# Kernel optimization log

Measured on AMD Instinct MI355X. Metric: run time of the kernel, lower is better.

## Reference

```python
import jax, jax.numpy as jnp
import numpy as np

NUM_CLASSES = 80
TOP_K = 200
CONF_T = 0.05
NMS_T = 0.5
CROP = 300.0
A = 49104
B = 8
NEG = -1.0  # dead-score sentinel; real scores are sigmoid outputs in (0,1)


def setup_inputs() -> dict:
    key = jax.random.key(0)
    k1, k2, k3, k4, k5, k6 = jax.random.split(key, 6)
    # structured, plausible anchors in (ymin, xmin, ymax, xmax), pixel coords
    yc = jax.random.uniform(k1, (A,)) * CROP
    xc = jax.random.uniform(k2, (A,)) * CROP
    h = 10.0 + jax.random.uniform(k5, (A,)) * 90.0
    w = 10.0 + jax.random.uniform(k6, (A,)) * 90.0
    anchors = jnp.stack([yc - h / 2, xc - w / 2, yc + h / 2, xc + w / 2], axis=-1)
    confidences = jax.random.normal(k3, (B, A, NUM_CLASSES + 1), dtype=jnp.float32)
    regressions = jax.random.normal(k4, (B, A, 4), dtype=jnp.float32) * 0.1
    return {"confidences": confidences, "regressions": regressions, "anchors": anchors}


def _decode(regressions, anchors):
    yca = (anchors[:, 0] + anchors[:, 2]) / 2
    xca = (anchors[:, 1] + anchors[:, 3]) / 2
    ha = anchors[:, 2] - anchors[:, 0]
    wa = anchors[:, 3] - anchors[:, 1]
    w = jnp.exp(regressions[..., 3]) * wa
    h = jnp.exp(regressions[..., 2]) * ha
    yc = regressions[..., 0] * ha + yca
    xc = regressions[..., 1] * wa + xca
    # clamp exactly as the original: min-clamp on xmin/ymin, max-clamp on xmax/ymax
    xmin = jnp.maximum(xc - w / 2, 0.0) / CROP
    ymin = jnp.maximum(yc - h / 2, 0.0) / CROP
    xmax = jnp.minimum(xc + w / 2, CROP - 1.0) / CROP
    ymax = jnp.minimum(yc + h / 2, CROP - 1.0) / CROP
    return jnp.stack([xmin, ymin, xmax, ymax], axis=-1)  # [B,A,4] (x1,y1,x2,y2)


def _iou_one_to_many(box, boxes):
    x1 = jnp.maximum(box[0], boxes[:, 0])
    y1 = jnp.maximum(box[1], boxes[:, 1])
    x2 = jnp.minimum(box[2], boxes[:, 2])
    y2 = jnp.minimum(box[3], boxes[:, 3])
    inter = jnp.maximum(x2 - x1, 0.0) * jnp.maximum(y2 - y1, 0.0)
    area_b = (box[2] - box[0]) * (box[3] - box[1])
    areas = (boxes[:, 2] - boxes[:, 0]) * (boxes[:, 3] - boxes[:, 1])
    union = area_b + areas - inter
    return jnp.where(union > 0, inter / union, 0.0)


def _nms_image(boxes, probs):
    # boxes: [A,4], probs: [A,C] (sigmoid, background stripped)
    scores = jnp.max(probs, axis=1)
    classes = jnp.argmax(probs, axis=1)
    valid = scores > CONF_T
    # batched_nms trick: offset boxes per class so cross-class IoU is 0
    offset = classes.astype(boxes.dtype) * (jnp.max(boxes) + 1.0)
    boxes_o = boxes + offset[:, None]
    live = jnp.where(valid, scores, NEG)

    def body(live, _):
        idx = jnp.argmax(live)
        keep = live[idx] > 0.0
        iou = _iou_one_to_many(boxes_o[idx], boxes_o)
        live = jnp.where(keep & (iou > NMS_T), NEG, live)
        live = live.at[idx].set(NEG)
        return live, (idx, keep)

    _, (idxs, keeps) = jax.lax.scan(body, live, None, length=TOP_K)
    cls_k = classes[idxs]          # [TOP_K]
    sc_k = scores[idxs]            # [TOP_K]
    bx_k = boxes[idxs]             # [TOP_K,4]
    # per-class slot = rank among kept detections of the same class (keep order is score-descending)
    onehot = (cls_k[:, None] == jnp.arange(NUM_CLASSES)[None, :]) & keeps[:, None]
    slot = jnp.cumsum(onehot, axis=0)[jnp.arange(TOP_K), cls_k] - 1
    rows = jnp.where(keeps, cls_k + 1, NUM_CLASSES + 1)  # OOB row when dropped
    slot = jnp.where(keeps, slot, TOP_K)                 # OOB col when dropped
    vals = jnp.concatenate([sc_k[:, None], bx_k], axis=1)  # [TOP_K,5]
    out = jnp.zeros((NUM_CLASSES + 1, TOP_K, 5), boxes.dtype)
    return out.at[rows, slot].set(vals, mode="drop")


def reference(confidences, regressions, anchors):
    probs = jax.nn.sigmoid(confidences[:, :, 1:])
    boxes = _decode(regressions, anchors)
    return jax.vmap(_nms_image)(boxes, probs)  # [B, C+1, TOP_K, 5]
```

## Files before the change

kernel.cpp:

```cpp
#include <hip/hip_runtime.h>
#include <stdint.h>

#define NCLS 80
#define TOPK 200
#define CONF_T 0.05f
#define CONF_BITS 0x3D4CCCCDu
#define CROPF 300.0f
#define NA 49104
#define NB 8
#define NSEL 256
#define MKEYS 4096
#define APB 64
#define T1 256
#define CHUNK (APB * 81)
#define NGRP (NA / 16)
#define MROW 5
#define OUTFLO ((NCLS + 1) * TOPK * 5)
#define NBLK1 ((NB * NA) / APB)
#define BASE13 125542u
#define NBINS 4512

__device__ __forceinline__ void decode_box(const float4 rg, const float4 an,
                                           float& x1, float& y1, float& x2, float& y2) {
    float yca = (an.x + an.z) * 0.5f;
    float xca = (an.y + an.w) * 0.5f;
    float ha = an.z - an.x;
    float wa = an.w - an.y;
    float w = expf(rg.w) * wa;
    float h = expf(rg.z) * ha;
    float yc = rg.x * ha + yca;
    float xc = rg.y * wa + xca;
    x1 = fmaxf(xc - w * 0.5f, 0.0f) / CROPF;
    y1 = fmaxf(yc - h * 0.5f, 0.0f) / CROPF;
    x2 = fminf(xc + w * 0.5f, CROPF - 1.0f) / CROPF;
    y2 = fminf(yc + h * 0.5f, CROPF - 1.0f) / CROPF;
}

__device__ __forceinline__ float rlf(float v, int l) {
    return __int_as_float(__builtin_amdgcn_readlane(__float_as_int(v), l));
}

__global__ __launch_bounds__(T1) void phase1_kernel(
    const float* __restrict__ conf, const float* __restrict__ reg,
    const float* __restrict__ anch, unsigned long long* __restrict__ key64,
    float4* __restrict__ boxes, float2* __restrict__ gm2,
    float* __restrict__ outz)
{
    __shared__ float lds[CHUNK];
    const int blk = blockIdx.x, t = threadIdx.x;

    {
        const int gid = blk * T1 + t;
        constexpr int TOT4 = NB * OUTFLO / 4;
        if (gid < TOT4)
            reinterpret_cast<float4*>(outz)[gid] = make_float4(0.f, 0.f, 0.f, 0.f);
    }

    const float4* src = reinterpret_cast<const float4*>(conf + (size_t)blk * CHUNK);
    float4* dst = reinterpret_cast<float4*>(lds);
    for (int i = t; i < CHUNK / 4; i += T1) dst[i] = src[i];
    __syncthreads();

    const int la = t >> 2, sub = t & 3;
    const int quad = blk * APB + la;
    const float* crow = lds + la * 81;
    float best = -3.0e38f; int bc = 255;
    #pragma unroll
    for (int k = 0; k < 20; ++k) {
        int c = 1 + sub + 4 * k;
        float v = crow[c];
        if (v > best) { best = v; bc = c; }
    }
    for (int m = 1; m <= 2; m <<= 1) {
        float ov = __shfl_xor(best, m);
        int oc = __shfl_xor(bc, m);
        if (ov > best || (ov == best && oc < bc)) { best = ov; bc = oc; }
    }
    unsigned long long key = 0ull;
    float bmaxl = 0.0f;
    if (sub == 0) {
        int a = quad % NA;
        float s = 1.0f / (1.0f + expf(-best));
        uint32_t ginv = 0x1FFFFu - (uint32_t)a;
        key = ((unsigned long long)__float_as_uint(s) << 32)
            | (unsigned long long)((ginv << 7) | (uint32_t)(bc - 1));
        float4 rg = reinterpret_cast<const float4*>(reg)[quad];
        float4 an = reinterpret_cast<const float4*>(anch)[a];
        float x1, y1, x2, y2; decode_box(rg, an, x1, y1, x2, y2);
        boxes[quad] = make_float4(x1, y1, x2, y2);
        bmaxl = fmaxf(fmaxf(x1, y1), fmaxf(x2, y2));
    }
    {
        const int lane = t & 63, w = t >> 6;
        unsigned long long kk = __shfl(key, (lane & 15) * 4);
        if (lane < 16)
            key64[(size_t)blk * APB + w * 16 + lane] = kk;
    }
    float wbest = best;
    #pragma unroll
    for (int m = 1; m < 64; m <<= 1) {
        wbest = fmaxf(wbest, __shfl_xor(wbest, m));
        bmaxl = fmaxf(bmaxl, __shfl_xor(bmaxl, m));
    }
    if ((t & 63) == 0)
        gm2[blk * 4 + (t >> 6)] = make_float2(1.0f / (1.0f + expf(-wbest)), bmaxl);
}

__device__ __forceinline__ void suffix_scan_1024(uint32_t v, int t,
                                                 uint32_t* wtot, uint32_t* outarr) {
    uint32_t r = v;
    const int lane = t & 63, w = t >> 6;
    #pragma unroll
    for (int m = 1; m < 64; m <<= 1) {
        uint32_t o = __shfl_down(r, m);
        if (lane + m < 64) r += o;
    }
    if (lane == 0) wtot[w] = r;
    __syncthreads();
    if (t < 16) {
        uint32_t v0 = wtot[t], x = v0;
        #pragma unroll
        for (int m = 1; m < 16; m <<= 1) {
            uint32_t o = __shfl_down(x, m);
            if (t + m < 16) x += o;
        }
        wtot[t] = x - v0;
    }
    __syncthreads();
    outarr[t] = r + wtot[w];
    __syncthreads();
}

__global__ __launch_bounds__(1024) void phase2_kernel(
    const unsigned long long* __restrict__ key64, const float4* __restrict__ boxes,
    const float2* __restrict__ gm2, float* __restrict__ out)
{
    __shared__ uint64_t s_keys[MKEYS];
    __shared__ uint64_t s_skeys[MKEYS];
    __shared__ uint64_t s_mask[256 * MROW];
    __shared__ float4   s_boxo[256];
    __shared__ float4   s_braw[256];
    __shared__ float    s_areao[256];
    __shared__ float    s_gm[NGRP + 3];
    __shared__ uint32_t s_glist[2048];
    __shared__ float4   s_keptbox[TOPK];
    __shared__ uint64_t s_clsmask[NCLS][4];
    __shared__ uint32_t s_ccount[NCLS];
    __shared__ uint32_t s_wtot[16];
    __shared__ uint32_t s_shv[12];
    __shared__ float    s_bmaxarr[16];
    __shared__ float    s_offm;
    __shared__ uint8_t  s_clsl[256];
    __shared__ uint64_t s_K[4];

    uint32_t* hist = (uint32_t*)s_keys;
    uint32_t* csum = (uint32_t*)s_skeys;

    const int b = blockIdx.x;
    const int t = threadIdx.x;

    for (int i = t; i < NBINS; i += 1024) hist[i] = 0;
    if (t < 12) s_shv[t] = 0;
    __syncthreads();

    {
        const float2* gmb = gm2 + (size_t)b * NGRP;
        float wm = 0.0f;
        for (int i = t; i < NGRP; i += 1024) {
            float2 v = gmb[i];
            s_gm[i] = v.x;
            wm = fmaxf(wm, v.y);
            if (v.x > CONF_T) {
                int ib = (int)((__float_as_uint(v.x) >> 13) - BASE13);
                ib = max(0, min(NBINS - 1, ib));
                atomicAdd(&hist[ib], 1u);
            }
        }
        #pragma unroll
        for (int m = 1; m < 64; m <<= 1) wm = fmaxf(wm, __shfl_xor(wm, m));
        if ((t & 63) == 0) s_bmaxarr[t >> 6] = wm;
    }
    __syncthreads();

    uint32_t v8 = 0;
    if (t * 8 < NBINS) {
        #pragma unroll
        for (int k = 0; k < 8; ++k) v8 += hist[t * 8 + k];
    }
    suffix_scan_1024(v8, t, s_wtot, csum);
    {
        uint32_t sIn = csum[t];
        uint32_t sNext = (t == 1023) ? 0u : csum[t + 1];
        if (sIn >= NSEL && sNext < NSEL) { s_shv[0] = (uint32_t)t; s_shv[1] = sNext; s_shv[2] = 1; }
    }
    __syncthreads();
    if (t == 0) {
        float mx = s_bmaxarr[0];
        #pragma unroll
        for (int k = 1; k < 16; ++k) mx = fmaxf(mx, s_bmaxarr[k]);
        s_offm = mx + 1.0f;
        if (s_shv[2]) {
            uint32_t chunk = s_shv[0], run2 = s_shv[1]; int cb = -1;
            for (int k = 7; k >= 0; --k) {
                uint32_t v = hist[chunk * 8 + k];
                if (cb < 0 && run2 + v >= NSEL) cb = (int)(chunk * 8 + k);
                run2 += v;
            }
            s_shv[3] = BASE13 + (uint32_t)cb;
        } else s_shv[3] = 0;
    }
    __syncthreads();

    const uint32_t T13 = s_shv[3];
    for (int i = t; i < NGRP; i += 1024) {
        float s = s_gm[i];
        if (s > CONF_T && (__float_as_uint(s) >> 13) >= T13) {
            uint32_t p = atomicAdd(&s_shv[8], 1u);
            if (p < 2048u) s_glist[p] = (uint32_t)i;
        }
    }
    __syncthreads();
    uint32_t ngl = s_shv[8]; if (ngl > 2048u) ngl = 2048u;

    {
        const unsigned long long* kb = key64 + (size_t)b * NA;
        for (int idx = t; idx < (int)(ngl * 16); idx += 1024) {
            uint32_t gi = s_glist[idx >> 4];
            unsigned long long key = kb[gi * 16 + (idx & 15)];
            uint32_t bits = (uint32_t)(key >> 32);
            if (bits > CONF_BITS && (bits >> 13) >= T13) {
                uint32_t p = atomicAdd(&s_shv[4], 1u);
                if (p < MKEYS) s_keys[p] = key;
            }
        }
    }
    __syncthreads();
    uint32_t nGa = s_shv[4]; if (nGa > MKEYS) nGa = MKEYS;
    const int lim = (nGa < 256u) ? (int)nGa : 256;

    {
        const int lane = t & 63;
        const uint32_t nch = (nGa + 63) >> 6;
        for (int s = 0; s < 4; ++s) {
            int kid = t + s * 1024;
            bool act = kid < (int)nGa;
            if (__ballot(act) == 0ull) continue;
            uint64_t my = act ? s_keys[kid] : ~0ull;
            uint32_t r = 0;
            for (uint32_t ch = 0; ch < nch; ++ch) {
                uint32_t src = ch * 64 + (uint32_t)lane;
                uint64_t kc = (src < nGa) ? s_keys[src] : 0ull;
                uint32_t clo = (uint32_t)kc, chi = (uint32_t)(kc >> 32);
                for (int jj = 0; jj < 64; ++jj) {
                    uint32_t olo = (uint32_t)__builtin_amdgcn_readlane((int)clo, jj);
                    uint32_t ohi = (uint32_t)__builtin_amdgcn_readlane((int)chi, jj);
                    uint64_t ok = ((uint64_t)ohi << 32) | olo;
                    r += (ok > my) ? 1u : 0u;
                }
            }
            if (act) s_skeys[r] = my;
        }
    }
    __syncthreads();

    const float offm = s_offm;
    if (t < 256) {
        if (t < lim) {
            uint64_t key = s_skeys[t];
            uint32_t low = (uint32_t)key;
            int c = (int)(low & 0x7Fu);
            uint32_t g = 0x1FFFFu - (low >> 7);
            s_clsl[t] = (uint8_t)c;
            float4 br = boxes[(size_t)b * NA + g];
            s_braw[t] = br;
            float off = (float)c * offm;
            float4 bo = make_float4(br.x + off, br.y + off, br.z + off, br.w + off);
            s_boxo[t] = bo;
            s_areao[t] = (bo.z - bo.x) * (bo.w - bo.y);
        } else {
            s_clsl[t] = 0;
            s_braw[t] = make_float4(0.f, 0.f, 0.f, 0.f);
            s_boxo[t] = make_float4(0.f, 0.f, 0.f, 0.f);
            s_areao[t] = 0.f;
        }
    }
    if (t < NCLS * 4) ((uint64_t*)s_clsmask)[t] = 0ull;
    __syncthreads();

    {
        const int wv = t >> 6, lane = t & 63;
        const int rbase = (wv & 3) * 64, c = wv >> 2;
        const int i = rbase + lane;
        float4 bi = s_boxo[i];
        float aI = s_areao[i];
        float4 vj = s_boxo[c * 64 + lane];
        float vA = s_areao[c * 64 + lane];
        uint64_t m = 0ull;
        for (int jj = 0; jj < 64; ++jj) {
            float bx1 = rlf(vj.x, jj), by1 = rlf(vj.y, jj);
            float bx2 = rlf(vj.z, jj), by2 = rlf(vj.w, jj);
            float aJ  = rlf(vA, jj);
            float ix1 = fmaxf(bi.x, bx1), iy1 = fmaxf(bi.y, by1);
            float ix2 = fminf(bi.z, bx2), iy2 = fminf(bi.w, by2);
            float inter = fmaxf(ix2 - ix1, 0.f) * fmaxf(iy2 - iy1, 0.f);
            float uni = aI + aJ - inter;
            if (uni > 0.f && inter + inter > uni) m |= (1ull << jj);
        }
        s_mask[(size_t)i * MROW + c] = m;
    }
    __syncthreads();

    if (t < 64) {
        const int lane = t;
        uint64_t mr[4][4];
        #pragma unroll
        for (int wr = 0; wr < 4; ++wr)
            #pragma unroll
            for (int wc = 0; wc < 4; ++wc)
                mr[wr][wc] = s_mask[(size_t)(wr * 64 + lane) * MROW + wc];
        const uint64_t below = (lane == 0) ? 0ull : ((~0ull) >> (64 - lane));
        uint64_t K[4];
        #pragma unroll
        for (int w = 0; w < 4; ++w) {
            int lo = w * 64, n = lim - lo;
            K[w] = (n >= 64) ? ~0ull : (n > 0 ? ((~0ull) >> (64 - n)) : 0ull);
        }
        for (int round = 0; round < 257; ++round) {
            uint64_t nK[4];
            #pragma unroll
            for (int wr = 0; wr < 4; ++wr) {
                uint64_t dead = 0ull;
                #pragma unroll
                for (int w = 0; w < 4; ++w) {
                    uint64_t mm = mr[wr][w] & K[w];
                    if (w < wr) dead |= mm;
                    else if (w == wr) dead |= (mm & below);
                }
                bool nb = (dead == 0ull) && (wr * 64 + lane < lim);
                nK[wr] = __ballot(nb);
            }
            bool same = (nK[0] == K[0]) && (nK[1] == K[1]) &&
                        (nK[2] == K[2]) && (nK[3] == K[3]);
            K[0] = nK[0]; K[1] = nK[1]; K[2] = nK[2]; K[3] = nK[3];
            if (same) break;
        }
        if (lane < 4) s_K[lane] = K[lane];
    }
    __syncthreads();

    if (t < 256 && ((s_K[(t >> 6) & 3] >> (t & 63)) & 1ull))
        atomicOr(&s_clsmask[s_clsl[t]][(t >> 6) & 3], 1ull << (t & 63));
    __syncthreads();
    if (t < NCLS) {
        uint32_t n = 0;
        #pragma unroll
        for (int w = 0; w < 4; ++w) n += (uint32_t)__popcll(s_clsmask[t][w]);
        s_ccount[t] = n;
    }
    if (t == 0) {
        uint32_t n = 0;
        #pragma unroll
        for (int w = 0; w < 4; ++w) n += (uint32_t)__popcll(s_K[w]);
        s_shv[7] = n;
    }
    __syncthreads();

    {
        const int jw = (t >> 6) & 3, jb = t & 63;
        bool kept = (t < 256) && ((s_K[jw] >> jb) & 1ull);
        if (kept) {
            const uint64_t below = (jb == 0) ? 0ull : ((~0ull) >> (64 - jb));
            uint32_t ord = (uint32_t)__popcll(s_K[jw] & below);
            for (int w = 0; w < jw; ++w) ord += (uint32_t)__popcll(s_K[w]);
            if (ord < TOPK) {
                int c = (int)s_clsl[t];
                const uint64_t* cm = s_clsmask[c];
                uint32_t slot = (uint32_t)__popcll(cm[jw] & below);
                for (int w = 0; w < jw; ++w) slot += (uint32_t)__popcll(cm[w]);
                float scv = __uint_as_float((uint32_t)(s_skeys[t] >> 32));
                float4 br = s_braw[t];
                float* o = out + (((size_t)b * (NCLS + 1) + (size_t)(c + 1)) * TOPK + slot) * 5;
                o[0] = scv; o[1] = br.x; o[2] = br.y; o[3] = br.z; o[4] = br.w;
                s_keptbox[ord] = s_boxo[t];
            }
        }
    }
    __syncthreads();

    if (t == 0) {
        uint32_t nk = s_shv[7];
        if (nk < TOPK && nGa > (uint32_t)lim) {
            for (uint32_t ci = (uint32_t)lim; ci < nGa && nk < TOPK; ++ci) {
                uint64_t key = s_skeys[ci];
                uint32_t low = (uint32_t)key;
                int c = (int)(low & 0x7Fu);
                uint32_t g = 0x1FFFFu - (low >> 7);
                float4 br = boxes[(size_t)b * NA + g];
                float off = (float)c * offm;
                float4 bo = make_float4(br.x + off, br.y + off, br.z + off, br.w + off);
                float aB2 = (bo.z - bo.x) * (bo.w - bo.y);
                bool sup = false;
                for (uint32_t k2 = 0; k2 < nk && !sup; ++k2) {
                    float4 kb = s_keptbox[k2];
                    float aK = (kb.z - kb.x) * (kb.w - kb.y);
                    float ix1 = fmaxf(bo.x, kb.x), iy1 = fmaxf(bo.y, kb.y);
                    float ix2 = fminf(bo.z, kb.z), iy2 = fminf(bo.w, kb.w);
                    float inter = fmaxf(ix2 - ix1, 0.f) * fmaxf(iy2 - iy1, 0.f);
                    float uni = aB2 + aK - inter;
                    sup = (uni > 0.f && inter + inter > uni);
                }
                if (!sup) {
                    uint32_t slot = s_ccount[c]; s_ccount[c] = slot + 1;
                    float scv = __uint_as_float((uint32_t)(key >> 32));
                    float* o = out + (((size_t)b * (NCLS + 1) + (size_t)(c + 1)) * TOPK + slot) * 5;
                    o[0] = scv; o[1] = br.x; o[2] = br.y; o[3] = br.z; o[4] = br.w;
                    s_keptbox[nk] = bo;
                    ++nk;
                }
            }
        }
    }
}

extern "C" void kernel_launch(void* const* d_in, const int* in_sizes, int n_in,
                              void* d_out, int out_size, void* d_ws, size_t ws_size,
                              hipStream_t stream)
{
    const float* conf = (const float*)d_in[0];
    const float* reg  = (const float*)d_in[1];
    const float* anch = (const float*)d_in[2];
    float* out = (float*)d_out;

    char* ws = (char*)d_ws;
    unsigned long long* key64 = (unsigned long long*)ws;
    float4* boxes = (float4*)(ws + (size_t)NB * NA * 8);
    float2* gm2 = (float2*)(ws + (size_t)NB * NA * 24);

    phase1_kernel<<<NBLK1, T1, 0, stream>>>(conf, reg, anch, key64, boxes, gm2, out);
    phase2_kernel<<<NB, 1024, 0, stream>>>(key64, boxes, gm2, out);
}
```

Before: 63.82 us.

## Speculatively compact high-score candidates in phase1 with fixed threshold, skipping histogram select

Phase1 now uses a wave ballot to write keys whose score is at or above a fixed threshold into a per-group compacted list, and stores the per-group count alongside the group max. Phase2 prefix-scans these counts and, when the total falls between the minimum selection size and the key buffer capacity, copies the keys straight into shared memory. This skips the histogram, threshold search, group filtering and key gather passes. If the count is out of range, it falls back to the original histogram path. Per-class counts are now computed only inside the serial fallback. The fixed threshold is tuned to the expected score distribution, and phase1 does extra writes.

```diff
diff --git a/kernel.cpp b/kernel.cpp
--- a/kernel.cpp
+++ b/kernel.cpp
@@ -5,6 +5,7 @@
 #define TOPK 200
 #define CONF_T 0.05f
 #define CONF_BITS 0x3D4CCCCDu
+#define TFIX 0.9775f
 #define CROPF 300.0f
 #define NA 49104
 #define NB 8
@@ -43,8 +44,8 @@
 __global__ __launch_bounds__(T1) void phase1_kernel(
     const float* __restrict__ conf, const float* __restrict__ reg,
     const float* __restrict__ anch, unsigned long long* __restrict__ key64,
-    float4* __restrict__ boxes, float2* __restrict__ gm2,
-    float* __restrict__ outz)
+    float4* __restrict__ boxes, float4* __restrict__ gmi,
+    unsigned long long* __restrict__ speclist, float* __restrict__ outz)
 {
     __shared__ float lds[CHUNK];
     const int blk = blockIdx.x, t = threadIdx.x;
@@ -77,12 +78,12 @@
         if (ov > best || (ov == best && oc < bc)) { best = ov; bc = oc; }
     }
     unsigned long long key = 0ull;
-    float bmaxl = 0.0f;
+    float bmaxl = 0.0f, sflt = -1.0f;
     if (sub == 0) {
         int a = quad % NA;
-        float s = 1.0f / (1.0f + expf(-best));
+        sflt = 1.0f / (1.0f + expf(-best));
         uint32_t ginv = 0x1FFFFu - (uint32_t)a;
-        key = ((unsigned long long)__float_as_uint(s) << 32)
+        key = ((unsigned long long)__float_as_uint(sflt) << 32)
             | (unsigned long long)((ginv << 7) | (uint32_t)(bc - 1));
         float4 rg = reinterpret_cast<const float4*>(reg)[quad];
         float4 an = reinterpret_cast<const float4*>(anch)[a];
@@ -96,6 +97,17 @@
         if (lane < 16)
             key64[(size_t)blk * APB + w * 16 + lane] = kk;
     }
+    uint32_t gcnt;
+    {
+        const int lane = t & 63;
+        bool qual = (sub == 0) && (sflt >= TFIX);
+        uint64_t qm = __ballot(qual);
+        gcnt = (uint32_t)__popcll(qm);
+        if (qual) {
+            uint32_t rank = (uint32_t)__popcll(qm & ((1ull << lane) - 1ull));
+            speclist[(size_t)(blk * 4 + (t >> 6)) * 16 + rank] = key;
+        }
+    }
     float wbest = best;
     #pragma unroll
     for (int m = 1; m < 64; m <<= 1) {
@@ -103,7 +115,8 @@
         bmaxl = fmaxf(bmaxl, __shfl_xor(bmaxl, m));
     }
     if ((t & 63) == 0)
-        gm2[blk * 4 + (t >> 6)] = make_float2(1.0f / (1.0f + expf(-wbest)), bmaxl);
+        gmi[blk * 4 + (t >> 6)] = make_float4(1.0f / (1.0f + expf(-wbest)), bmaxl,
+                                              __uint_as_float(gcnt), 0.0f);
 }
 
 __device__ __forceinline__ void suffix_scan_1024(uint32_t v, int t,
@@ -133,19 +146,20 @@
 
 __global__ __launch_bounds__(1024) void phase2_kernel(
     const unsigned long long* __restrict__ key64, const float4* __restrict__ boxes,
-    const float2* __restrict__ gm2, float* __restrict__ out)
+    const float4* __restrict__ gmi, const unsigned long long* __restrict__ speclist,
+    float* __restrict__ out)
 {
     __shared__ uint64_t s_keys[MKEYS];
     __shared__ uint64_t s_skeys[MKEYS];
+    __shared__ float    s_gm[NGRP + 3];
     __shared__ uint64_t s_mask[256 * MROW];
     __shared__ float4   s_boxo[256];
     __shared__ float4   s_braw[256];
     __shared__ float    s_areao[256];
-    __shared__ float    s_gm[NGRP + 3];
-    __shared__ uint32_t s_glist[2048];
     __shared__ float4   s_keptbox[TOPK];
     __shared__ uint64_t s_clsmask[NCLS][4];
     __shared__ uint32_t s_ccount[NCLS];
+    __shared__ uint32_t s_glist[2048];
     __shared__ uint32_t s_wtot[16];
     __shared__ uint32_t s_shv[12];
     __shared__ float    s_bmaxarr[16];
@@ -159,89 +173,114 @@
     const int b = blockIdx.x;
     const int t = threadIdx.x;
 
-    for (int i = t; i < NBINS; i += 1024) hist[i] = 0;
     if (t < 12) s_shv[t] = 0;
     __syncthreads();
 
-    {
-        const float2* gmb = gm2 + (size_t)b * NGRP;
+    uint32_t c0 = 0, c1 = 0, c2 = 0;
+    {
+        const float4* gmb = gmi + (size_t)b * NGRP;
         float wm = 0.0f;
-        for (int i = t; i < NGRP; i += 1024) {
-            float2 v = gmb[i];
+        int k = 0;
+        for (int i = t; i < NGRP; i += 1024, ++k) {
+            float4 v = gmb[i];
             s_gm[i] = v.x;
             wm = fmaxf(wm, v.y);
-            if (v.x > CONF_T) {
-                int ib = (int)((__float_as_uint(v.x) >> 13) - BASE13);
+            uint32_t c = __float_as_uint(v.z);
+            if (k == 0) c0 = c; else if (k == 1) c1 = c; else c2 = c;
+        }
+        #pragma unroll
+        for (int m = 1; m < 64; m <<= 1) wm = fmaxf(wm, __shfl_xor(wm, m));
+        if ((t & 63) == 0) s_bmaxarr[t >> 6] = wm;
+    }
+    suffix_scan_1024(c0 + c1 + c2, t, s_wtot, csum);
+    const uint32_t mysuf = csum[t];
+    const uint32_t total = csum[0];
+    if (t == 0) {
+        float mx = s_bmaxarr[0];
+        #pragma unroll
+        for (int k = 1; k < 16; ++k) mx = fmaxf(mx, s_bmaxarr[k]);
+        s_offm = mx + 1.0f;
+        s_shv[5] = (total >= NSEL && total <= MKEYS) ? 1u : 0u;
+        s_shv[4] = total;
+    }
+    __syncthreads();
+
+    const bool fastp = (s_shv[5] != 0);
+    if (fastp) {
+        const unsigned long long* sp = speclist + (size_t)b * NA;
+        uint32_t p = total - mysuf;
+        for (uint32_t j = 0; j < c0; ++j) s_keys[p++] = sp[(size_t)t * 16 + j];
+        for (uint32_t j = 0; j < c1; ++j) s_keys[p++] = sp[(size_t)(t + 1024) * 16 + j];
+        for (uint32_t j = 0; j < c2; ++j) s_keys[p++] = sp[(size_t)(t + 2048) * 16 + j];
+        __syncthreads();
+    } else {
+        for (int i = t; i < NBINS; i += 1024) hist[i] = 0;
+        if (t == 0) s_shv[4] = 0;
+        __syncthreads();
+        for (int i = t; i < NGRP; i += 1024) {
+            float s = s_gm[i];
+            if (s > CONF_T) {
+                int ib = (int)((__float_as_uint(s) >> 13) - BASE13);
                 ib = max(0, min(NBINS - 1, ib));
                 atomicAdd(&hist[ib], 1u);
             }
         }
-        #pragma unroll
-        for (int m = 1; m < 64; m <<= 1) wm = fmaxf(wm, __shfl_xor(wm, m));
-        if ((t & 63) == 0) s_bmaxarr[t >> 6] = wm;
-    }
-    __syncthreads();
-
-    uint32_t v8 = 0;
-    if (t * 8 < NBINS) {
-        #pragma unroll
-        for (int k = 0; k < 8; ++k) v8 += hist[t * 8 + k];
-    }
-    suffix_scan_1024(v8, t, s_wtot, csum);
-    {
-        uint32_t sIn = csum[t];
-        uint32_t sNext = (t == 1023) ? 0u : csum[t + 1];
-        if (sIn >= NSEL && sNext < NSEL) { s_shv[0] = (uint32_t)t; s_shv[1] = sNext; s_shv[2] = 1; }
-    }
-    __syncthreads();
-    if (t == 0) {
-        float mx = s_bmaxarr[0];
-        #pragma unroll
-        for (int k = 1; k < 16; ++k) mx = fmaxf(mx, s_bmaxarr[k]);
-        s_offm = mx + 1.0f;
-        if (s_shv[2]) {
-            uint32_t chunk = s_shv[0], run2 = s_shv[1]; int cb = -1;
-            for (int k = 7; k >= 0; --k) {
-                uint32_t v = hist[chunk * 8 + k];
-                if (cb < 0 && run2 + v >= NSEL) cb = (int)(chunk * 8 + k);
-                run2 += v;
-            }
-            s_shv[3] = BASE13 + (uint32_t)cb;
-        } else s_shv[3] = 0;
-    }
-    __syncthreads();
-
-    const uint32_t T13 = s_shv[3];
-    for (int i = t; i < NGRP; i += 1024) {
-        float s = s_gm[i];
-        if (s > CONF_T && (__float_as_uint(s) >> 13) >= T13) {
-            uint32_t p = atomicAdd(&s_shv[8], 1u);
-            if (p < 2048u) s_glist[p] = (uint32_t)i;
-        }
-    }
-    __syncthreads();
-    uint32_t ngl = s_shv[8]; if (ngl > 2048u) ngl = 2048u;
-
-    {
-        const unsigned long long* kb = key64 + (size_t)b * NA;
-        for (int idx = t; idx < (int)(ngl * 16); idx += 1024) {
-            uint32_t gi = s_glist[idx >> 4];
-            unsigned long long key = kb[gi * 16 + (idx & 15)];
-            uint32_t bits = (uint32_t)(key >> 32);
-            if (bits > CONF_BITS && (bits >> 13) >= T13) {
-                uint32_t p = atomicAdd(&s_shv[4], 1u);
-                if (p < MKEYS) s_keys[p] = key;
-            }
-        }
-    }
-    __syncthreads();
+        __syncthreads();
+        uint32_t v8 = 0;
+        if (t * 8 < NBINS) {
+            #pragma unroll
+            for (int k = 0; k < 8; ++k) v8 += hist[t * 8 + k];
+        }
+        suffix_scan_1024(v8, t, s_wtot, csum);
+        {
+            uint32_t sIn = csum[t];
+            uint32_t sNext = (t == 1023) ? 0u : csum[t + 1];
+            if (sIn >= NSEL && sNext < NSEL) { s_shv[0] = (uint32_t)t; s_shv[1] = sNext; s_shv[2] = 1; }
+        }
+        __syncthreads();
+        if (t == 0) {
+            if (s_shv[2]) {
+                uint32_t chunk = s_shv[0], run2 = s_shv[1]; int cb = -1;
+                for (int k = 7; k >= 0; --k) {
+                    uint32_t v = hist[chunk * 8 + k];
+                    if (cb < 0 && run2 + v >= NSEL) cb = (int)(chunk * 8 + k);
+                    run2 += v;
+                }
+                s_shv[3] = BASE13 + (uint32_t)cb;
+            } else s_shv[3] = 0;
+        }
+        __syncthreads();
+        const uint32_t T13 = s_shv[3];
+        for (int i = t; i < NGRP; i += 1024) {
+            float s = s_gm[i];
+            if (s > CONF_T && (__float_as_uint(s) >> 13) >= T13) {
+                uint32_t p = atomicAdd(&s_shv[8], 1u);
+                if (p < 2048u) s_glist[p] = (uint32_t)i;
+            }
+        }
+        __syncthreads();
+        uint32_t ngl = s_shv[8]; if (ngl > 2048u) ngl = 2048u;
+        {
+            const unsigned long long* kb = key64 + (size_t)b * NA;
+            for (int idx = t; idx < (int)(ngl * 16); idx += 1024) {
+                uint32_t gi = s_glist[idx >> 4];
+                unsigned long long key = kb[gi * 16 + (idx & 15)];
+                uint32_t bits = (uint32_t)(key >> 32);
+                if (bits > CONF_BITS && (bits >> 13) >= T13) {
+                    uint32_t p = atomicAdd(&s_shv[4], 1u);
+                    if (p < MKEYS) s_keys[p] = key;
+                }
+            }
+        }
+        __syncthreads();
+    }
     uint32_t nGa = s_shv[4]; if (nGa > MKEYS) nGa = MKEYS;
     const int lim = (nGa < 256u) ? (int)nGa : 256;
 
     {
         const int lane = t & 63;
         const uint32_t nch = (nGa + 63) >> 6;
-        for (int s = 0; s < 4; ++s) {
+        for (int s = 0; s < MKEYS / 1024; ++s) {
             int kid = t + s * 1024;
             bool act = kid < (int)nGa;
             if (__ballot(act) == 0ull) continue;
@@ -351,19 +390,6 @@
     if (t < 256 && ((s_K[(t >> 6) & 3] >> (t & 63)) & 1ull))
         atomicOr(&s_clsmask[s_clsl[t]][(t >> 6) & 3], 1ull << (t & 63));
     __syncthreads();
-    if (t < NCLS) {
-        uint32_t n = 0;
-        #pragma unroll
-        for (int w = 0; w < 4; ++w) n += (uint32_t)__popcll(s_clsmask[t][w]);
-        s_ccount[t] = n;
-    }
-    if (t == 0) {
-        uint32_t n = 0;
-        #pragma unroll
-        for (int w = 0; w < 4; ++w) n += (uint32_t)__popcll(s_K[w]);
-        s_shv[7] = n;
-    }
-    __syncthreads();
 
     {
         const int jw = (t >> 6) & 3, jb = t & 63;
@@ -388,8 +414,16 @@
     __syncthreads();
 
     if (t == 0) {
-        uint32_t nk = s_shv[7];
+        uint32_t nk = 0;
+        #pragma unroll
+        for (int w = 0; w < 4; ++w) nk += (uint32_t)__popcll(s_K[w]);
         if (nk < TOPK && nGa > (uint32_t)lim) {
+            for (int c = 0; c < NCLS; ++c) {
+                uint32_t n = 0;
+                #pragma unroll
+                for (int w = 0; w < 4; ++w) n += (uint32_t)__popcll(s_clsmask[c][w]);
+                s_ccount[c] = n;
+            }
             for (uint32_t ci = (uint32_t)lim; ci < nGa && nk < TOPK; ++ci) {
                 uint64_t key = s_skeys[ci];
                 uint32_t low = (uint32_t)key;
@@ -434,8 +468,12 @@
     char* ws = (char*)d_ws;
     unsigned long long* key64 = (unsigned long long*)ws;
     float4* boxes = (float4*)(ws + (size_t)NB * NA * 8);
-    float2* gm2 = (float2*)(ws + (size_t)NB * NA * 24);
-
-    phase1_kernel<<<NBLK1, T1, 0, stream>>>(conf, reg, anch, key64, boxes, gm2, out);
-    phase2_kernel<<<NB, 1024, 0, stream>>>(key64, boxes, gm2, out);
-}
+    float4* gmi   = (float4*)(ws + (size_t)NB * NA * 24);
+    unsigned long long* speclist =
+        (unsigned long long*)(ws + (size_t)NB * NA * 24
+                                 + (size_t)NB * NGRP * 16);
+
+    phase1_kernel<<<NBLK1, T1, 0, stream>>>(conf, reg, anch, key64, boxes,
+                                            gmi, speclist, out);
+    phase2_kernel<<<NB, 1024, 0, stream>>>(key64, boxes, gmi, speclist, out);
+}
```

Measured after the change: 63.57 us. About the same (-0.4%).
